# Kernel tuning notes

Measured on AMD Instinct MI355X. Metric: run time of the kernel, lower is better.

The kernel has to match this reference:

```python
import jax, jax.numpy as jnp
import numpy as np

E = 8          # num_experts
T = 16384      # total tokens (sum of expert_size)
D = 1024       # d_model
F = 4096       # d_ff


def setup_inputs() -> dict:
    key = jax.random.key(0)
    k_x, k_w1, k_w2 = jax.random.split(key, 3)
    s1 = 1.0 / np.sqrt(D)
    s2 = 1.0 / np.sqrt(F)
    return {
        "inputs": jax.random.normal(k_x, (T, D), dtype=jnp.float32),
        # equal-sized per-expert chunks (reference assumes uniform routing)
        "expert_size": jnp.full((E,), T // E, dtype=jnp.int32),
        "w1": jax.random.normal(k_w1, (E, D, F), dtype=jnp.float32) * s1,
        "b1": jnp.zeros((E, F), dtype=jnp.float32),
        "w2": jax.random.normal(k_w2, (E, F, D), dtype=jnp.float32) * s2,
        "b2": jnp.zeros((E, D), dtype=jnp.float32),
    }


def reference(inputs, expert_size, w1, b1, w2, b2):
    """ParallelExperts forward: split tokens by expert_size, run each expert
    (Linear->GELU->Linear), concat. With equal chunk sizes the split+loop+concat
    is exactly a grouped (batched-per-expert) GEMM, expressed here as one
    reshape + batched einsum instead of a Python loop of small matmuls."""
    e = w1.shape[0]
    t, d = inputs.shape
    x = inputs.reshape(e, t // e, d)                      # [E, T/E, D]
    h = jax.nn.gelu(jnp.einsum('etd,edf->etf', x, w1) + b1[:, None, :])
    y = jnp.einsum('etf,efd->etd', h, w2) + b2[:, None, :]
    return y.reshape(t, d)
```

## Files before the change

### kernel.cpp

```cpp
#include <hip/hip_runtime.h>

typedef unsigned short ushort_t;
typedef __attribute__((ext_vector_type(8))) unsigned short ushortx8;
typedef __attribute__((ext_vector_type(8))) __bf16 bf16x8;
typedef __attribute__((ext_vector_type(4))) float floatx4;

#define NE 8
#define NT 16384
#define ND 1024
#define NF 4096
#define MPE (NT / NE)

__device__ __forceinline__ float b2f(ushort_t x) {
    unsigned u = ((unsigned)x) << 16;
    float f;
    __builtin_memcpy(&f, &u, 4);
    return f;
}
__device__ __forceinline__ ushort_t f2b(float f) {
    unsigned u;
    __builtin_memcpy(&u, &f, 4);
    u += 0x7FFFu + ((u >> 16) & 1u);
    return (ushort_t)(u >> 16);
}
__device__ __forceinline__ float gelu_tanh(float x) {
    float u = x + 0.044715f * x * x * x;
    float e = __expf(1.5957691216f * u);
    float t = 1.0f - 2.0f / (e + 1.0f);
    return 0.5f * x * (1.0f + t);
}

__global__ void detect_dtype(const ushort_t* __restrict__ x, int* __restrict__ flag) {
    int l = threadIdx.x;
    float v = b2f(x[2 * l]);
    float a = fabsf(v);
    int big = (a > 1e4f) || (a != a);
    unsigned long long m = __ballot(big);
    if (l == 0) *flag = (__popcll(m) >= 4) ? 1 : 0;
}

__global__ __launch_bounds__(256) void conv_bf16(
    const void* __restrict__ src, ushort_t* __restrict__ dst, int n,
    const int* __restrict__ flagp)
{
    int flag = *flagp;
    int i = (blockIdx.x * 256 + threadIdx.x) * 8;
    if (i >= n) return;
    if (flag) {
        const float* s = (const float*)src + i;
        ushortx8 o;
#pragma unroll
        for (int j = 0; j < 8; ++j) o[j] = f2b(s[j]);
        *(ushortx8*)(dst + i) = o;
    } else {
        *(ushortx8*)(dst + i) = *(const ushortx8*)((const ushort_t*)src + i);
    }
}

__global__ __launch_bounds__(256) void transpose_e(
    const void* __restrict__ src, ushort_t* __restrict__ dst, int R, int C,
    const int* __restrict__ flagp)
{
    __shared__ ushort_t tile[64][72];
    int flag = *flagp;
    int e = blockIdx.z;
    size_t ebase = (size_t)e * R * C;
    int r0 = blockIdx.y * 64, c0 = blockIdx.x * 64;
    int t = threadIdx.x;
#pragma unroll
    for (int i = 0; i < 2; ++i) {
        int ch = t + 256 * i;
        int r = ch >> 3;
        int c = (ch & 7) * 8;
        size_t gi = ebase + (size_t)(r0 + r) * C + (c0 + c);
        ushortx8 v;
        if (flag) {
            const float* s = (const float*)src + gi;
#pragma unroll
            for (int j = 0; j < 8; ++j) v[j] = f2b(s[j]);
        } else {
            v = *(const ushortx8*)((const ushort_t*)src + gi);
        }
        *(ushortx8*)&tile[r][c] = v;
    }
    __syncthreads();
#pragma unroll
    for (int i = 0; i < 2; ++i) {
        int ch = t + 256 * i;
        int oc  = ch >> 3;
        int orr = (ch & 7) * 8;
        ushortx8 v;
#pragma unroll
        for (int j = 0; j < 8; ++j) v[j] = tile[orr + j][oc];
        *(ushortx8*)(dst + ebase + (size_t)(c0 + oc) * R + (r0 + orr)) = v;
    }
}

template <int GELU, int DUALOUT>
__global__ __launch_bounds__(256) void gemm_bt(
    const ushort_t* __restrict__ A, const ushort_t* __restrict__ Bt,
    const ushort_t* __restrict__ bias, void* __restrict__ Cout,
    int Mpe, int N, int K, const int* __restrict__ flagp)
{
    __shared__ __align__(16) ushort_t sA[128 * 64];
    __shared__ __align__(16) ushort_t sB[128 * 64];

    const int flag = DUALOUT ? *flagp : 0;
    const int e  = blockIdx.z;
    const int m0 = blockIdx.y * 128;
    const int n0 = blockIdx.x * 128;
    const ushort_t* Ae = A  + (size_t)e * Mpe * K + (size_t)m0 * K;
    const ushort_t* Be = Bt + (size_t)e * N   * K + (size_t)n0 * K;

    const int t = threadIdx.x;
    const int w = t >> 6;
    const int l = t & 63;
    const int lwr = l >> 3;
    const int swz = (l & 7) ^ lwr;
    const int q  = l >> 4;
    const int ln = l & 15;

    floatx4 acc[4][4] = {};

    for (int kt = 0; kt < K; kt += 64) {
#pragma unroll
        for (int it = 0; it < 4; ++it) {
            int rb = it * 32 + w * 8;
            const ushort_t* ga = Ae + (size_t)(rb + lwr) * K + kt + swz * 8;
            __builtin_amdgcn_global_load_lds(
                (const __attribute__((address_space(1))) void*)ga,
                (__attribute__((address_space(3))) void*)&sA[rb * 64], 16, 0, 0);
            const ushort_t* gb = Be + (size_t)(rb + lwr) * K + kt + swz * 8;
            __builtin_amdgcn_global_load_lds(
                (const __attribute__((address_space(1))) void*)gb,
                (__attribute__((address_space(3))) void*)&sB[rb * 64], 16, 0, 0);
        }
        __syncthreads();
#pragma unroll
        for (int ks = 0; ks < 2; ++ks) {
            bf16x8 af[4], bfr[4];
#pragma unroll
            for (int mt = 0; mt < 4; ++mt) {
                int m = (w >> 1) * 64 + mt * 16 + ln;
                af[mt] = *(const bf16x8*)&sA[m * 64 + (((ks * 4 + q) ^ (m & 7)) * 8)];
            }
#pragma unroll
            for (int nt = 0; nt < 4; ++nt) {
                int n = (w & 1) * 64 + nt * 16 + ln;
                bfr[nt] = *(const bf16x8*)&sB[n * 64 + (((ks * 4 + q) ^ (n & 7)) * 8)];
            }
#pragma unroll
            for (int mt = 0; mt < 4; ++mt)
#pragma unroll
                for (int nt = 0; nt < 4; ++nt)
                    acc[mt][nt] = __builtin_amdgcn_mfma_f32_16x16x32_bf16(
                        af[mt], bfr[nt], acc[mt][nt], 0, 0, 0);
        }
        __syncthreads();
    }

    const ushort_t* be = bias + (size_t)e * N + n0;
#pragma unroll
    for (int nt = 0; nt < 4; ++nt) {
        int col = (w & 1) * 64 + nt * 16 + ln;
        float bv = b2f(be[col]);
#pragma unroll
        for (int mt = 0; mt < 4; ++mt) {
#pragma unroll
            for (int r = 0; r < 4; ++r) {
                int row = (w >> 1) * 64 + mt * 16 + q * 4 + r;
                float v = acc[mt][nt][r] + bv;
                if (GELU) v = gelu_tanh(v);
                size_t idx = (size_t)e * Mpe * N + (size_t)(m0 + row) * N + (n0 + col);
                if (DUALOUT && flag) ((float*)Cout)[idx] = v;
                else                 ((ushort_t*)Cout)[idx] = f2b(v);
            }
        }
    }
}

extern "C" void kernel_launch(void* const* d_in, const int* in_sizes, int n_in,
                              void* d_out, int out_size, void* d_ws, size_t ws_size,
                              hipStream_t stream) {
    const void* x  = d_in[0];
    const void* w1 = d_in[2];
    const void* b1 = d_in[3];
    const void* w2 = d_in[4];
    const void* b2 = d_in[5];

    char* ws = (char*)d_ws;
    int*      flag = (int*)ws;
    ushort_t* xb   = (ushort_t*)(ws + ((size_t)1  << 20));
    ushort_t* b1b  = (ushort_t*)(ws + ((size_t)34 << 20));
    ushort_t* b2b  = (ushort_t*)(ws + ((size_t)35 << 20));
    ushort_t* wT   = (ushort_t*)(ws + ((size_t)36 << 20));
    ushort_t* H    = (ushort_t*)(ws + ((size_t)100 << 20));

    detect_dtype<<<1, 64, 0, stream>>>((const ushort_t*)x, flag);

    conv_bf16<<<(NT * ND / 8 + 255) / 256, 256, 0, stream>>>(x,  xb,  NT * ND, flag);
    conv_bf16<<<(NE * NF / 8 + 255) / 256, 256, 0, stream>>>(b1, b1b, NE * NF, flag);
    conv_bf16<<<(NE * ND / 8 + 255) / 256, 256, 0, stream>>>(b2, b2b, NE * ND, flag);

    transpose_e<<<dim3(NF / 64, ND / 64, NE), 256, 0, stream>>>(w1, wT, ND, NF, flag);
    gemm_bt<1, 0><<<dim3(NF / 128, MPE / 128, NE), 256, 0, stream>>>(
        xb, wT, b1b, H, MPE, NF, ND, flag);
    transpose_e<<<dim3(ND / 64, NF / 64, NE), 256, 0, stream>>>(w2, wT, NF, ND, flag);
    gemm_bt<0, 1><<<dim3(ND / 128, MPE / 128, NE), 256, 0, stream>>>(
        H, wT, b2b, d_out, MPE, ND, NF, flag);
}
```

Measured before the change: 801.4 us.

## Use 256x256 double-buffered 8-wave GEMM with interleaved prefetch; swizzle transpose tile

```diff
diff --git a/kernel.cpp b/kernel.cpp
--- a/kernel.cpp
+++ b/kernel.cpp
@@ -61,7 +61,7 @@
     const void* __restrict__ src, ushort_t* __restrict__ dst, int R, int C,
     const int* __restrict__ flagp)
 {
-    __shared__ ushort_t tile[64][72];
+    __shared__ __align__(16) ushort_t tile[64 * 64];
     int flag = *flagp;
     int e = blockIdx.z;
     size_t ebase = (size_t)e * R * C;
@@ -70,9 +70,9 @@
 #pragma unroll
     for (int i = 0; i < 2; ++i) {
         int ch = t + 256 * i;
-        int r = ch >> 3;
-        int c = (ch & 7) * 8;
-        size_t gi = ebase + (size_t)(r0 + r) * C + (c0 + c);
+        int r  = ch >> 3;
+        int c8 = ch & 7;
+        size_t gi = ebase + (size_t)(r0 + r) * C + (c0 + c8 * 8);
         ushortx8 v;
         if (flag) {
             const float* s = (const float*)src + gi;
@@ -81,99 +81,164 @@
         } else {
             v = *(const ushortx8*)((const ushort_t*)src + gi);
         }
-        *(ushortx8*)&tile[r][c] = v;
+        *(ushortx8*)&tile[r * 64 + ((c8 ^ ((r >> 3) & 7)) * 8)] = v;
     }
     __syncthreads();
 #pragma unroll
     for (int i = 0; i < 2; ++i) {
-        int ch = t + 256 * i;
+        int ch  = t + 256 * i;
         int oc  = ch >> 3;
         int orr = (ch & 7) * 8;
         ushortx8 v;
 #pragma unroll
-        for (int j = 0; j < 8; ++j) v[j] = tile[orr + j][oc];
+        for (int j = 0; j < 8; ++j) {
+            int rr = orr + j;
+            v[j] = tile[rr * 64 + (((oc >> 3) ^ ((rr >> 3) & 7)) * 8) + (oc & 7)];
+        }
         *(ushortx8*)(dst + ebase + (size_t)(c0 + oc) * R + (r0 + orr)) = v;
     }
 }
 
 template <int GELU, int DUALOUT>
-__global__ __launch_bounds__(256) void gemm_bt(
+__global__ __launch_bounds__(512, 2) void gemm_bt8(
     const ushort_t* __restrict__ A, const ushort_t* __restrict__ Bt,
     const ushort_t* __restrict__ bias, void* __restrict__ Cout,
     int Mpe, int N, int K, const int* __restrict__ flagp)
 {
-    __shared__ __align__(16) ushort_t sA[128 * 64];
-    __shared__ __align__(16) ushort_t sB[128 * 64];
+    __shared__ __align__(16) ushort_t sA[2][256 * 64];
+    __shared__ __align__(16) ushort_t sB[2][256 * 64];
 
     const int flag = DUALOUT ? *flagp : 0;
     const int e  = blockIdx.z;
-    const int m0 = blockIdx.y * 128;
-    const int n0 = blockIdx.x * 128;
+    const int m0 = blockIdx.y * 256;
+    const int n0 = blockIdx.x * 256;
     const ushort_t* Ae = A  + (size_t)e * Mpe * K + (size_t)m0 * K;
     const ushort_t* Be = Bt + (size_t)e * N   * K + (size_t)n0 * K;
 
-    const int t = threadIdx.x;
-    const int w = t >> 6;
-    const int l = t & 63;
+    const int t  = threadIdx.x;
+    const int w  = t >> 6;
+    const int l  = t & 63;
+    const int wr = w >> 2;
+    const int wc = w & 3;
     const int lwr = l >> 3;
     const int swz = (l & 7) ^ lwr;
     const int q  = l >> 4;
     const int ln = l & 15;
 
-    floatx4 acc[4][4] = {};
-
-    for (int kt = 0; kt < K; kt += 64) {
-#pragma unroll
-        for (int it = 0; it < 4; ++it) {
-            int rb = it * 32 + w * 8;
-            const ushort_t* ga = Ae + (size_t)(rb + lwr) * K + kt + swz * 8;
-            __builtin_amdgcn_global_load_lds(
-                (const __attribute__((address_space(1))) void*)ga,
-                (__attribute__((address_space(3))) void*)&sA[rb * 64], 16, 0, 0);
-            const ushort_t* gb = Be + (size_t)(rb + lwr) * K + kt + swz * 8;
-            __builtin_amdgcn_global_load_lds(
-                (const __attribute__((address_space(1))) void*)gb,
-                (__attribute__((address_space(3))) void*)&sB[rb * 64], 16, 0, 0);
-        }
-        __syncthreads();
-#pragma unroll
-        for (int ks = 0; ks < 2; ++ks) {
-            bf16x8 af[4], bfr[4];
-#pragma unroll
-            for (int mt = 0; mt < 4; ++mt) {
-                int m = (w >> 1) * 64 + mt * 16 + ln;
-                af[mt] = *(const bf16x8*)&sA[m * 64 + (((ks * 4 + q) ^ (m & 7)) * 8)];
-            }
-#pragma unroll
-            for (int nt = 0; nt < 4; ++nt) {
-                int n = (w & 1) * 64 + nt * 16 + ln;
-                bfr[nt] = *(const bf16x8*)&sB[n * 64 + (((ks * 4 + q) ^ (n & 7)) * 8)];
-            }
-#pragma unroll
-            for (int mt = 0; mt < 4; ++mt)
-#pragma unroll
-                for (int nt = 0; nt < 4; ++nt)
-                    acc[mt][nt] = __builtin_amdgcn_mfma_f32_16x16x32_bf16(
-                        af[mt], bfr[nt], acc[mt][nt], 0, 0, 0);
-        }
-        __syncthreads();
-    }
+    const int KT = K >> 6;
+
+#define STAGE(G, S, r0c, kcol) do {                                          \
+        int rb_ = (r0c) + w * 8;                                             \
+        const ushort_t* ga_ = (G) + (size_t)(rb_ + lwr) * K + (kcol) + swz * 8; \
+        __builtin_amdgcn_global_load_lds(                                    \
+            (const __attribute__((address_space(1))) void*)ga_,              \
+            (__attribute__((address_space(3))) void*)&(S)[rb_ * 64], 16, 0, 0); \
+    } while (0)
+
+    floatx4 acc[8][4] = {};
+
+    STAGE(Ae, sA[0],   0, 0); STAGE(Ae, sA[0],  64, 0);
+    STAGE(Ae, sA[0], 128, 0); STAGE(Ae, sA[0], 192, 0);
+    STAGE(Be, sB[0],   0, 0); STAGE(Be, sB[0],  64, 0);
+    STAGE(Be, sB[0], 128, 0); STAGE(Be, sB[0], 192, 0);
+    if (KT > 1) {
+        STAGE(Ae, sA[1],   0, 64);
+        STAGE(Ae, sA[1], 128, 64);
+        asm volatile("s_waitcnt vmcnt(2)" ::: "memory");
+    } else {
+        asm volatile("s_waitcnt vmcnt(0)" ::: "memory");
+    }
+    __builtin_amdgcn_s_barrier();
+
+    for (int kt = 0; kt < KT; ++kt) {
+        const int cur = kt & 1;
+        ushort_t* sAc = &sA[cur][0];
+        ushort_t* sBc = &sB[cur][0];
+        ushort_t* sAn = &sA[cur ^ 1][0];
+        ushort_t* sBn = &sB[cur ^ 1][0];
+        const int kc = kt * 64;
+
+#pragma unroll
+        for (int p = 0; p < 4; ++p) {
+            const int qm = p >> 1, qn = p & 1;
+
+            bf16x8 af[2][4], bv[2][2];
+#pragma unroll
+            for (int ks = 0; ks < 2; ++ks) {
+#pragma unroll
+                for (int mi = 0; mi < 4; ++mi) {
+                    int m = wr * 128 + qm * 64 + mi * 16 + ln;
+                    af[ks][mi] = *(const bf16x8*)&sAc[m * 64 + (((ks * 4 + q) ^ (m & 7)) * 8)];
+                }
+#pragma unroll
+                for (int nj = 0; nj < 2; ++nj) {
+                    int n = wc * 64 + qn * 32 + nj * 16 + ln;
+                    bv[ks][nj] = *(const bf16x8*)&sBc[n * 64 + (((ks * 4 + q) ^ (n & 7)) * 8)];
+                }
+            }
+
+            if (p == 0 && kt + 1 < KT) {
+                STAGE(Ae, sAn,  64, kc + 64);
+                STAGE(Ae, sAn, 192, kc + 64);
+                STAGE(Be, sBn,   0, kc + 64);
+                STAGE(Be, sBn,  64, kc + 64);
+            }
+            if (p == 1 && kt + 1 < KT) {
+                STAGE(Be, sBn, 128, kc + 64);
+                STAGE(Be, sBn, 192, kc + 64);
+            }
+            if (p == 2 && kt + 2 < KT) {
+                STAGE(Ae, sAc,   0, kc + 128);
+                STAGE(Ae, sAc, 128, kc + 128);
+            }
+
+            __builtin_amdgcn_s_barrier();
+            asm volatile("s_waitcnt lgkmcnt(0)" ::: "memory");
+            __builtin_amdgcn_sched_barrier(0);
+
+            __builtin_amdgcn_s_setprio(1);
+#pragma unroll
+            for (int ks = 0; ks < 2; ++ks)
+#pragma unroll
+                for (int mi = 0; mi < 4; ++mi)
+#pragma unroll
+                    for (int nj = 0; nj < 2; ++nj)
+                        acc[qm * 4 + mi][qn * 2 + nj] =
+                            __builtin_amdgcn_mfma_f32_16x16x32_bf16(
+                                af[ks][mi], bv[ks][nj],
+                                acc[qm * 4 + mi][qn * 2 + nj], 0, 0, 0);
+            __builtin_amdgcn_s_setprio(0);
+
+            if (p == 3) {
+                if (kt + 2 < KT) asm volatile("s_waitcnt vmcnt(2)" ::: "memory");
+                else             asm volatile("s_waitcnt vmcnt(0)" ::: "memory");
+            }
+            __builtin_amdgcn_s_barrier();
+        }
+    }
+#undef STAGE
 
     const ushort_t* be = bias + (size_t)e * N + n0;
 #pragma unroll
-    for (int nt = 0; nt < 4; ++nt) {
-        int col = (w & 1) * 64 + nt * 16 + ln;
-        float bv = b2f(be[col]);
-#pragma unroll
-        for (int mt = 0; mt < 4; ++mt) {
-#pragma unroll
-            for (int r = 0; r < 4; ++r) {
-                int row = (w >> 1) * 64 + mt * 16 + q * 4 + r;
-                float v = acc[mt][nt][r] + bv;
-                if (GELU) v = gelu_tanh(v);
-                size_t idx = (size_t)e * Mpe * N + (size_t)(m0 + row) * N + (n0 + col);
-                if (DUALOUT && flag) ((float*)Cout)[idx] = v;
-                else                 ((ushort_t*)Cout)[idx] = f2b(v);
+    for (int qn = 0; qn < 2; ++qn) {
+#pragma unroll
+        for (int nj = 0; nj < 2; ++nj) {
+            int col = wc * 64 + qn * 32 + nj * 16 + ln;
+            float bvv = b2f(be[col]);
+#pragma unroll
+            for (int qm = 0; qm < 2; ++qm) {
+#pragma unroll
+                for (int mi = 0; mi < 4; ++mi) {
+#pragma unroll
+                    for (int r = 0; r < 4; ++r) {
+                        int row = wr * 128 + qm * 64 + mi * 16 + q * 4 + r;
+                        float v = acc[qm * 4 + mi][qn * 2 + nj][r] + bvv;
+                        if (GELU) v = gelu_tanh(v);
+                        size_t idx = (size_t)e * Mpe * N + (size_t)(m0 + row) * N + (n0 + col);
+                        if (DUALOUT && flag) ((float*)Cout)[idx] = v;
+                        else                 ((ushort_t*)Cout)[idx] = f2b(v);
+                    }
+                }
             }
         }
     }
@@ -203,9 +268,9 @@
     conv_bf16<<<(NE * ND / 8 + 255) / 256, 256, 0, stream>>>(b2, b2b, NE * ND, flag);
 
     transpose_e<<<dim3(NF / 64, ND / 64, NE), 256, 0, stream>>>(w1, wT, ND, NF, flag);
-    gemm_bt<1, 0><<<dim3(NF / 128, MPE / 128, NE), 256, 0, stream>>>(
+    gemm_bt8<1, 0><<<dim3(NF / 256, MPE / 256, NE), 512, 0, stream>>>(
         xb, wT, b1b, H, MPE, NF, ND, flag);
     transpose_e<<<dim3(ND / 64, NF / 64, NE), 256, 0, stream>>>(w2, wT, NF, ND, flag);
-    gemm_bt<0, 1><<<dim3(ND / 128, MPE / 128, NE), 256, 0, stream>>>(
+    gemm_bt8<0, 1><<<dim3(ND / 256, MPE / 256, NE), 512, 0, stream>>>(
         H, wT, b2b, d_out, MPE, ND, NF, flag);
 }
```

Measured after the change: 767.0 us. 1.04x faster.
